# Kernel optimization log

Measured on AMD Instinct MI355X. Metric: run time of the kernel, lower is better.

## Reference

```python
import jax, jax.numpy as jnp
import numpy as np

S_, H_, W_ = 7, 56, 56   # input_resolution
WS = 7                   # window_size
SHIFT = 3                # shift_size
GT = 1                   # gt_num (global tokens per window)
HEADS = 12
EPS = 1e-5


def _rel_pos_index(w):
    # replicates the torch buffer construction (incl. its 3*w-1 / 2*w-1 multipliers)
    coords = np.stack(np.meshgrid(np.arange(w), np.arange(w), np.arange(w), indexing='ij'))
    cf = coords.reshape(3, -1)
    rc = (cf[:, :, None] - cf[:, None, :]).transpose(1, 2, 0).astype(np.int64)
    rc += w - 1
    rc[..., 0] *= 3 * w - 1
    rc[..., 1] *= 2 * w - 1
    return rc.sum(-1)  # (w^3, w^3)


def _attn_mask(S, H, W, w, sh):
    # standard 3D shifted-window mask, built once from static shapes
    img = np.zeros((S, H, W))
    cnt = 0
    sls = (slice(0, -w), slice(-w, -sh), slice(-sh, None))
    for a in sls:
        for b in sls:
            for c in sls:
                img[a, b, c] = cnt
                cnt += 1
    m = img.reshape(S // w, w, H // w, w, W // w, w).transpose(0, 2, 4, 1, 3, 5).reshape(-1, w ** 3)
    d = m[:, None, :] - m[:, :, None]
    return np.where(d != 0, -100.0, 0.0).astype(np.float32)  # (nW, w^3, w^3)


def _ln(x, g, b):
    mu = jnp.mean(x, -1, keepdims=True)
    var = jnp.mean((x - mu) ** 2, -1, keepdims=True)
    return (x - mu) * jax.lax.rsqrt(var + EPS) * g + b


def setup_inputs() -> dict:
    key = jax.random.key(0)
    ks = jax.random.split(key, 7)
    C = 384
    hid = 4 * C
    L = S_ * H_ * W_
    nW = (S_ // WS) * (H_ // WS) * (W_ // WS)
    p = lambda k, shape: jax.random.normal(k, shape, jnp.float32) * 0.02
    return dict(
        x=jax.random.normal(ks[0], (1, L, C), jnp.float32),
        gt=jax.random.normal(ks[1], (nW, GT, C), jnp.float32),
        norm1_g=jnp.ones((C,), jnp.float32), norm1_b=jnp.zeros((C,), jnp.float32),
        qkv_w=p(ks[2], (C, 3 * C)), qkv_b=jnp.zeros((3 * C,), jnp.float32),
        bias_table=p(ks[3], ((2 * WS - 1) ** 3, HEADS)),
        proj_w=p(ks[4], (C, C)), proj_b=jnp.zeros((C,), jnp.float32),
        norm2_g=jnp.ones((C,), jnp.float32), norm2_b=jnp.zeros((C,), jnp.float32),
        fc1_w=p(ks[5], (C, hid)), fc1_b=jnp.zeros((hid,), jnp.float32),
        fc2_w=p(ks[6], (hid, C)), fc2_b=jnp.zeros((C,), jnp.float32),
    )


def _forward(x, gt, norm1_g, norm1_b, qkv_w, qkv_b, bias_table, proj_w, proj_b,
             norm2_g, norm2_b, fc1_w, fc1_b, fc2_w, fc2_b):
    B, L, C = x.shape
    h = HEADS
    d = C // h
    scale = d ** -0.5
    N_ = WS ** 3
    N = N_ + GT
    rpi = _rel_pos_index(WS)
    mask = jnp.asarray(_attn_mask(S_, H_, W_, WS, SHIFT))
    nW = mask.shape[0]

    shortcut = x
    xs = _ln(x, norm1_g, norm1_b).reshape(B, S_, H_, W_, C)
    xs = jnp.roll(xs, (-SHIFT, -SHIFT, -SHIFT), axis=(1, 2, 3))  # cyclic shift
    # window partition -> (B*nW, N_, C)
    xw = xs.reshape(B, S_ // WS, WS, H_ // WS, WS, W_ // WS, WS, C)
    xw = xw.transpose(0, 1, 3, 5, 2, 4, 6, 7).reshape(-1, N_, C)

    # --- WindowAttention with global tokens ---
    xc = jnp.concatenate([gt, xw], axis=1)  # (B*nW, N, C)
    qkv = (xc @ qkv_w + qkv_b).reshape(-1, N, 3, h, d).transpose(2, 0, 3, 1, 4)
    q, k, v = qkv[0] * scale, qkv[1], qkv[2]  # (B*nW, h, N, d)
    attn = jnp.einsum('bhnd,bhmd->bhnm', q, k)
    bias = bias_table[rpi.reshape(-1)].reshape(N_, N_, h).transpose(2, 0, 1)  # (h, N_, N_)
    bias = jnp.pad(bias, ((0, 0), (GT, 0), (GT, 0)))      # zeros on gt rows/cols == original submatrix add
    mpad = jnp.pad(mask, ((0, 0), (GT, 0), (GT, 0)))
    attn = attn + bias[None]
    attn = attn.reshape(B, nW, h, N, N) + mpad[None, :, None]
    attn = jax.nn.softmax(attn.reshape(-1, h, N, N), axis=-1)
    out = jnp.einsum('bhnm,bhmd->bhnd', attn, v).transpose(0, 2, 1, 3).reshape(-1, N, C)
    out = out @ proj_w + proj_b
    gt_out = out[:, :GT]
    xw = out[:, GT:]

    # window reverse + reverse shift
    xs = xw.reshape(B, S_ // WS, H_ // WS, W_ // WS, WS, WS, WS, C)
    xs = xs.transpose(0, 1, 4, 2, 5, 3, 6, 7).reshape(B, S_, H_, W_, C)
    xs = jnp.roll(xs, (SHIFT, SHIFT, SHIFT), axis=(1, 2, 3)).reshape(B, L, C)

    x = shortcut + xs  # drop_path = 0
    y = _ln(x, norm2_g, norm2_b)
    y = jax.nn.gelu(y @ fc1_w + fc1_b, approximate=False) @ fc2_w + fc2_b
    return x + y, gt_out


def reference(x, gt, norm1_g, norm1_b, qkv_w, qkv_b, bias_table, proj_w, proj_b,
              norm2_g, norm2_b, fc1_w, fc1_b, fc2_w, fc2_b):
    return _forward(x, gt, norm1_g, norm1_b, qkv_w, qkv_b, bias_table, proj_w, proj_b,
                    norm2_g, norm2_b, fc1_w, fc1_b, fc2_w, fc2_b)
```

## Files before the change

kernel.cpp:

```cpp
#include <hip/hip_runtime.h>
#include <math.h>

typedef __attribute__((ext_vector_type(8))) short short8;
typedef __attribute__((ext_vector_type(4))) float f32x4;

__device__ __forceinline__ float b2f(short s) {
    unsigned u = ((unsigned)(unsigned short)s) << 16;
    return __builtin_bit_cast(float, u);
}
__device__ __forceinline__ short f2b(float f) {
    unsigned u = __builtin_bit_cast(unsigned, f);
    u += 0x7FFFu + ((u >> 16) & 1u);
    return (short)(u >> 16);
}
__device__ __forceinline__ void gload16(const void* g, void* l) {
    __builtin_amdgcn_global_load_lds(
        (const __attribute__((address_space(1))) unsigned int*)g,
        (__attribute__((address_space(3))) unsigned int*)l, 16, 0, 0);
}

__global__ void transpose_w(const float* __restrict__ src, short* __restrict__ dst,
                            int K, int N) {
    int idx = blockIdx.x * 256 + threadIdx.x;
    if (idx < N * K) {
        int n = idx / K, k = idx - n * K;
        dst[idx] = f2b(src[(size_t)k * N + n]);
    }
}

__global__ void bias_pre(const float* __restrict__ btab, float* __restrict__ btf) {
    int idx = blockIdx.x * 256 + threadIdx.x;
    if (idx >= 12 * 22 * 22 * 64) return;
    int lane = idx & 63, rem = idx >> 6;
    int nb = rem % 22; rem /= 22;
    int rt = rem % 22; int head = rem / 22;
    int j = nb * 16 + (lane & 15);
    int ibase = rt * 16 + (lane >> 4) * 4;
    f32x4 out;
    #pragma unroll
    for (int r = 0; r < 4; r++) {
        int i = ibase + r;
        float v;
        if (j >= 344) v = -1e30f;
        else if (i >= 344 || i == 0 || j == 0) v = 0.f;
        else {
            int ti = i - 1, tj = j - 1;
            int ai = ti / 49, bi = (ti % 49) / 7, ci = ti % 7;
            int aj = tj / 49, bj = (tj % 49) / 7, cj = tj % 7;
            int id3 = (ai - aj + 6) * 20 + (bi - bj + 6) * 13 + (ci - cj + 6);
            v = btab[id3 * 12 + head];
        }
        out[r] = v;
    }
    *(f32x4*)&btf[(size_t)idx * 4] = out;
}

__global__ void gid_pre(unsigned char* __restrict__ gid) {
    int idx = blockIdx.x * 256 + threadIdx.x;
    if (idx >= 64 * 352) return;
    int w = idx / 352, n = idx % 352;
    unsigned char g = 0;
    if (n >= 1 && n < 344) {
        int t = n - 1;
        int a = t / 49, bb = (t % 49) / 7, cc = t % 7;
        int hw = w >> 3, ww = w & 7;
        int h = hw * 7 + bb, wd = ww * 7 + cc;
        int gs = (a < 4) ? 1 : 2;
        int gh = (h < 49) ? 0 : ((h < 53) ? 1 : 2);
        int gw = (wd < 49) ? 0 : ((wd < 53) ? 1 : 2);
        g = (unsigned char)(gs * 9 + gh * 3 + gw);
    }
    gid[idx] = g;
}

__global__ __launch_bounds__(256) void ln1_window(
    const float* __restrict__ x, const float* __restrict__ gt,
    const float* __restrict__ g, const float* __restrict__ b,
    short* __restrict__ xc)
{
    int wid = threadIdx.x >> 6, lane = threadIdx.x & 63;
    int r = blockIdx.x * 4 + wid;
    int w = r / 344, n = r - w * 344;
    if (n == 0) {
        #pragma unroll
        for (int i = 0; i < 6; i++) {
            int c = lane + i * 64;
            xc[(size_t)r * 384 + c] = f2b(gt[(size_t)w * 384 + c]);
        }
        return;
    }
    int t = n - 1;
    int a = t / 49, rm = t - a * 49, bb = rm / 7, cc = rm - bb * 7;
    int hw = w >> 3, ww = w & 7;
    int s = (a < 4) ? a + 3 : a - 4;
    int h = hw * 7 + bb + 3; if (h >= 56) h -= 56;
    int wd = ww * 7 + cc + 3; if (wd >= 56) wd -= 56;
    const float* row = x + (size_t)((s * 56 + h) * 56 + wd) * 384;
    float v[6]; float sum = 0.f;
    #pragma unroll
    for (int i = 0; i < 6; i++) { v[i] = row[lane + i * 64]; sum += v[i]; }
    #pragma unroll
    for (int off = 32; off >= 1; off >>= 1) sum += __shfl_xor(sum, off);
    float mu = sum * (1.0f / 384.0f);
    float vs = 0.f;
    #pragma unroll
    for (int i = 0; i < 6; i++) { float d = v[i] - mu; vs += d * d; }
    #pragma unroll
    for (int off = 32; off >= 1; off >>= 1) vs += __shfl_xor(vs, off);
    float rstd = rsqrtf(vs * (1.0f / 384.0f) + 1e-5f);
    #pragma unroll
    for (int i = 0; i < 6; i++) {
        int c = lane + i * 64;
        float o = (v[i] - mu) * rstd * g[c] + b[c];
        xc[(size_t)r * 384 + c] = f2b(o);
    }
}

__global__ __launch_bounds__(256) void ln2_kernel(
    const float* __restrict__ xn, const float* __restrict__ g,
    const float* __restrict__ b, short* __restrict__ out)
{
    int wid = threadIdx.x >> 6, lane = threadIdx.x & 63;
    int r = blockIdx.x * 4 + wid;
    const float* row = xn + (size_t)r * 384;
    float v[6]; float sum = 0.f;
    #pragma unroll
    for (int i = 0; i < 6; i++) { v[i] = row[lane + i * 64]; sum += v[i]; }
    #pragma unroll
    for (int off = 32; off >= 1; off >>= 1) sum += __shfl_xor(sum, off);
    float mu = sum * (1.0f / 384.0f);
    float vs = 0.f;
    #pragma unroll
    for (int i = 0; i < 6; i++) { float d = v[i] - mu; vs += d * d; }
    #pragma unroll
    for (int off = 32; off >= 1; off >>= 1) vs += __shfl_xor(vs, off);
    float rstd = rsqrtf(vs * (1.0f / 384.0f) + 1e-5f);
    #pragma unroll
    for (int i = 0; i < 6; i++) {
        int c = lane + i * 64;
        float o = (v[i] - mu) * rstd * g[c] + b[c];
        out[(size_t)r * 384 + c] = f2b(o);
    }
}

template<int EPI, bool QS>
__global__ __launch_bounds__(256, 4) void gemm128(
    const short* __restrict__ A, const short* __restrict__ BT,
    const float* __restrict__ bias, void* __restrict__ Out,
    const void* __restrict__ P0, void* __restrict__ P1,
    int M, int N, int K)
{
    __shared__ short As[128 * 64];
    __shared__ short Bs[128 * 64];
    const int m0 = blockIdx.y * 128, n0 = blockIdx.x * 128;
    const int tid = threadIdx.x;
    const int wid = tid >> 6, lane = tid & 63;
    const int wm = wid >> 1, wn = wid & 1;
    const int l15 = lane & 15, quad = lane >> 4;

    f32x4 acc[4][4];
    #pragma unroll
    for (int i = 0; i < 4; i++)
        #pragma unroll
        for (int j = 0; j < 4; j++) acc[i][j] = (f32x4){0.f, 0.f, 0.f, 0.f};

    const int trow = tid >> 3;
    const int cs = tid & 7;
    const int gc = cs ^ (trow & 7);
    const short* Ag[4]; const short* Bg[4];
    #pragma unroll
    for (int j = 0; j < 4; j++) {
        int ar = m0 + j * 32 + trow; if (ar >= M) ar = M - 1;
        Ag[j] = A + (size_t)ar * K + gc * 8;
        Bg[j] = BT + (size_t)(n0 + j * 32 + trow) * K + gc * 8;
    }
    short* AsW[4]; short* BsW[4];
    #pragma unroll
    for (int j = 0; j < 4; j++) {
        AsW[j] = &As[(j * 32 + wid * 8) * 64];
        BsW[j] = &Bs[(j * 32 + wid * 8) * 64];
    }
    int arow[4], brow[4];
    #pragma unroll
    for (int mt = 0; mt < 4; mt++) arow[mt] = wm * 64 + mt * 16 + l15;
    #pragma unroll
    for (int nt = 0; nt < 4; nt++) brow[nt] = wn * 64 + nt * 16 + l15;

    for (int ks = 0; ks < K; ks += 64) {
        #pragma unroll
        for (int j = 0; j < 4; j++) gload16(Ag[j] + ks, AsW[j]);
        #pragma unroll
        for (int j = 0; j < 4; j++) gload16(Bg[j] + ks, BsW[j]);
        __syncthreads();
        #pragma unroll
        for (int ko = 0; ko < 2; ko++) {
            short8 af[4], bf[4];
            #pragma unroll
            for (int mt = 0; mt < 4; mt++)
                af[mt] = *(const short8*)&As[arow[mt] * 64
                         + (((ko * 4 + quad) ^ (l15 & 7)) * 8)];
            #pragma unroll
            for (int nt = 0; nt < 4; nt++)
                bf[nt] = *(const short8*)&Bs[brow[nt] * 64
                         + (((ko * 4 + quad) ^ (l15 & 7)) * 8)];
            #pragma unroll
            for (int mt = 0; mt < 4; mt++)
                #pragma unroll
                for (int nt = 0; nt < 4; nt++)
                    acc[mt][nt] = __builtin_amdgcn_mfma_f32_16x16x32_bf16(
                        af[mt], bf[nt], acc[mt][nt], 0, 0, 0);
        }
        __syncthreads();
    }

    #pragma unroll
    for (int mt = 0; mt < 4; mt++) {
        #pragma unroll
        for (int nt = 0; nt < 4; nt++) {
            #pragma unroll
            for (int r = 0; r < 4; r++) {
                int row = m0 + wm * 64 + mt * 16 + quad * 4 + r;
                int col = n0 + wn * 64 + nt * 16 + l15;
                if (row >= M) continue;
                float v = acc[mt][nt][r] + bias[col];
                if (EPI == 0) {
                    if (QS && col < 384) v *= 0.17677669529663687f;
                    ((short*)Out)[(size_t)row * N + col] = f2b(v);
                } else if (EPI == 1) {
                    v = 0.5f * v * (1.0f + erff(v * 0.7071067811865476f));
                    ((short*)Out)[(size_t)row * N + col] = f2b(v);
                } else if (EPI == 2) {
                    int w = row / 344, n = row - w * 344;
                    if (n == 0) {
                        ((float*)P1)[(size_t)w * 384 + col] = v;
                    } else {
                        int t = n - 1;
                        int a = t / 49, rm = t - a * 49;
                        int bb = rm / 7, cc = rm - bb * 7;
                        int hw = w >> 3, ww = w & 7;
                        int s = (a < 4) ? a + 3 : a - 4;
                        int h = hw * 7 + bb + 3; if (h >= 56) h -= 56;
                        int wd = ww * 7 + cc + 3; if (wd >= 56) wd -= 56;
                        size_t td = (size_t)((s * 56 + h) * 56 + wd) * 384 + col;
                        ((float*)Out)[td] = v + ((const float*)P0)[td];
                    }
                } else {
                    v += ((const float*)P0)[(size_t)row * N + col];
                    ((float*)Out)[(size_t)row * N + col] = v;
                }
            }
        }
    }
}

__global__ __launch_bounds__(256) void attn_kernel(
    const short* __restrict__ qkv, const float* __restrict__ btf,
    const unsigned char* __restrict__ gid, short* __restrict__ attn_out)
{
    __shared__ short KT[352 * 40];
    __shared__ short VT[32 * 360];
    __shared__ short Pbuf[4 * 16 * 40];
    __shared__ unsigned char Gs[352];
    const int blk = blockIdx.x;
    const int half = blk & 1, wh = blk >> 1;
    const int w = wh / 12, head = wh - w * 12;
    const int tid = threadIdx.x;
    const int wid = tid >> 6, lane = tid & 63;
    const int l15 = lane & 15, quad = lane >> 4;
    const size_t base = (size_t)w * 344 * 1152 + head * 32;

    for (int c = tid; c < 352 * 4; c += 256) {
        int row = c >> 2, off = (c & 3) * 8;
        short8 v8 = (short8){0,0,0,0,0,0,0,0};
        if (row < 344) v8 = *(const short8*)&qkv[base + 384 + (size_t)row * 1152 + off];
        *(short8*)&KT[row * 40 + off] = v8;
    }
    for (int e = tid; e < 344 * 32; e += 256) {
        int key = e >> 5, dd = e & 31;
        VT[dd * 360 + key] = qkv[base + 768 + (size_t)key * 1152 + dd];
    }
    for (int e = tid; e < 16 * 32; e += 256) {
        int key = 344 + (e >> 5), dd = e & 31;
        VT[dd * 360 + key] = 0;
    }
    for (int e = tid; e < 352; e += 256) Gs[e] = gid[w * 352 + e];
    __syncthreads();

    const float* bh = btf + (size_t)head * (22 * 22 * 256);
    short* Pw = &Pbuf[wid * 640];

    for (int rtl = wid; rtl < 11; rtl += 4) {
        int rt = half * 11 + rtl;
        int mbase = rt * 16;
        int qr = mbase + l15; if (qr > 343) qr = 343;
        short8 af = *(const short8*)&qkv[base + (size_t)qr * 1152 + quad * 8];

        int rg[4]; bool ip[4];
        #pragma unroll
        for (int r = 0; r < 4; r++) {
            int i = mbase + quad * 4 + r;
            rg[r] = Gs[i];
            ip[r] = (i > 0);
        }

        f32x4 o0 = {0.f, 0.f, 0.f, 0.f}, o1 = {0.f, 0.f, 0.f, 0.f};
        float l[4] = {0.f, 0.f, 0.f, 0.f};

        #pragma unroll
        for (int kk = 0; kk < 11; kk++) {
            int nb0 = kk * 2, nb1 = kk * 2 + 1;
            f32x4 b0 = *(const f32x4*)&bh[((size_t)(rt * 22 + nb0) * 64 + lane) * 4];
            f32x4 b1 = *(const f32x4*)&bh[((size_t)(rt * 22 + nb1) * 64 + lane) * 4];
            short8 k0 = *(const short8*)&KT[(nb0 * 16 + l15) * 40 + quad * 8];
            short8 k1 = *(const short8*)&KT[(nb1 * 16 + l15) * 40 + quad * 8];
            f32x4 s0 = __builtin_amdgcn_mfma_f32_16x16x32_bf16(af, k0, b0, 0, 0, 0);
            f32x4 s1 = __builtin_amdgcn_mfma_f32_16x16x32_bf16(af, k1, b1, 0, 0, 0);

            int j0 = nb0 * 16 + l15;
            int cg0 = Gs[j0], cg1 = Gs[j0 + 16];
            bool jp0 = (j0 > 0);
            #pragma unroll
            for (int r = 0; r < 4; r++) {
                float s0r = s0[r], s1r = s1[r];
                if (jp0 && ip[r] && rg[r] != cg0) s0r -= 100.0f;
                if (ip[r] && rg[r] != cg1) s1r -= 100.0f;
                float p0 = __expf(s0r);
                float p1 = __expf(s1r);
                l[r] += p0 + p1;
                Pw[(quad * 4 + r) * 40 + l15] = f2b(p0);
                Pw[(quad * 4 + r) * 40 + 16 + l15] = f2b(p1);
            }
            short8 pa = *(const short8*)&Pw[l15 * 40 + quad * 8];
            short8 v0 = *(const short8*)&VT[l15 * 360 + kk * 32 + quad * 8];
            short8 v1 = *(const short8*)&VT[(16 + l15) * 360 + kk * 32 + quad * 8];
            o0 = __builtin_amdgcn_mfma_f32_16x16x32_bf16(pa, v0, o0, 0, 0, 0);
            o1 = __builtin_amdgcn_mfma_f32_16x16x32_bf16(pa, v1, o1, 0, 0, 0);
        }

        #pragma unroll
        for (int r = 0; r < 4; r++) {
            l[r] += __shfl_xor(l[r], 1);
            l[r] += __shfl_xor(l[r], 2);
            l[r] += __shfl_xor(l[r], 4);
            l[r] += __shfl_xor(l[r], 8);
        }
        #pragma unroll
        for (int r = 0; r < 4; r++) {
            int row = mbase + quad * 4 + r;
            if (row < 344) {
                float inv = 1.0f / l[r];
                size_t ob = ((size_t)w * 344 + row) * 384 + head * 32;
                attn_out[ob + l15] = f2b(o0[r] * inv);
                attn_out[ob + 16 + l15] = f2b(o1[r] * inv);
            }
        }
    }
}

extern "C" void kernel_launch(void* const* d_in, const int* in_sizes, int n_in,
                              void* d_out, int out_size, void* d_ws, size_t ws_size,
                              hipStream_t stream)
{
    const float* x      = (const float*)d_in[0];
    const float* gt     = (const float*)d_in[1];
    const float* n1g    = (const float*)d_in[2];
    const float* n1b    = (const float*)d_in[3];
    const float* qkv_w  = (const float*)d_in[4];
    const float* qkv_b  = (const float*)d_in[5];
    const float* btab   = (const float*)d_in[6];
    const float* proj_w = (const float*)d_in[7];
    const float* proj_b = (const float*)d_in[8];
    const float* n2g    = (const float*)d_in[9];
    const float* n2b    = (const float*)d_in[10];
    const float* fc1_w  = (const float*)d_in[11];
    const float* fc1_b  = (const float*)d_in[12];
    const float* fc2_w  = (const float*)d_in[13];
    const float* fc2_b  = (const float*)d_in[14];

    char* ws = (char*)d_ws;
    short* wt_qkv  = (short*)(ws + 0);
    short* wt_proj = (short*)(ws + 884736);
    short* wt_fc1  = (short*)(ws + 1179648);
    short* wt_fc2  = (short*)(ws + 2359296);
    short* xc      = (short*)(ws + 3538944);
    short* qkvb    = (short*)(ws + 20447232);
    short* attn_o  = xc;
    short* h1      = (short*)(ws + 3538944);
    float* xnew    = (float*)(ws + 71172096);
    float* btf     = (float*)(ws + 71172096);
    unsigned char* gidb = (unsigned char*)(ws + 77119488);
    short* xnorm   = (short*)(ws + 104890368);

    float* outx  = (float*)d_out;
    float* outgt = outx + (size_t)21952 * 384;

    transpose_w<<<dim3((442368 + 255) / 256), 256, 0, stream>>>(qkv_w, wt_qkv, 384, 1152);
    transpose_w<<<dim3((147456 + 255) / 256), 256, 0, stream>>>(proj_w, wt_proj, 384, 384);
    transpose_w<<<dim3((589824 + 255) / 256), 256, 0, stream>>>(fc1_w, wt_fc1, 384, 1536);
    transpose_w<<<dim3((589824 + 255) / 256), 256, 0, stream>>>(fc2_w, wt_fc2, 1536, 384);

    bias_pre<<<dim3((12 * 22 * 22 * 64 + 255) / 256), 256, 0, stream>>>(btab, btf);
    gid_pre<<<dim3((64 * 352 + 255) / 256), 256, 0, stream>>>(gidb);

    ln1_window<<<dim3(5504), 256, 0, stream>>>(x, gt, n1g, n1b, xc);

    gemm128<0, true><<<dim3(9, 172), 256, 0, stream>>>(xc, wt_qkv, qkv_b, qkvb,
                                                       nullptr, nullptr, 22016, 1152, 384);

    attn_kernel<<<dim3(1536), 256, 0, stream>>>(qkvb, btf, gidb, attn_o);

    gemm128<2, false><<<dim3(3, 172), 256, 0, stream>>>(attn_o, wt_proj, proj_b, xnew,
                                                        x, outgt, 22016, 384, 384);

    ln2_kernel<<<dim3(5488), 256, 0, stream>>>(xnew, n2g, n2b, xnorm);

    gemm128<1, false><<<dim3(12, 172), 256, 0, stream>>>(xnorm, wt_fc1, fc1_b, h1,
                                                         nullptr, nullptr, 21952, 1536, 384);

    gemm128<3, false><<<dim3(3, 172), 256, 0, stream>>>(h1, wt_fc2, fc2_b, outx,
                                                        xnew, nullptr, 21952, 384, 1536);
}
```

Measured before the change: 441.6 us.

## Tile weight transposes via LDS, raise GEMM occupancy, use tanh-form GELU

The weight transpose kernel now goes through a 32x32 LDS tile, so both reads and writes are coalesced instead of strided. The GEMM launch bounds now ask for 5 waves-per-SIMD occupancy instead of 4, which may cap registers and cause spills. The fc1 epilogue replaces exact erf GELU with a tanh-approximation written as x*sigmoid using fast exp and rcp. This lowers epilogue cost but departs from the exact GELU the reference requires.

```diff
diff --git a/kernel.cpp b/kernel.cpp
--- a/kernel.cpp
+++ b/kernel.cpp
@@ -19,12 +19,24 @@
         (__attribute__((address_space(3))) unsigned int*)l, 16, 0, 0);
 }
 
-__global__ void transpose_w(const float* __restrict__ src, short* __restrict__ dst,
-                            int K, int N) {
-    int idx = blockIdx.x * 256 + threadIdx.x;
-    if (idx < N * K) {
-        int n = idx / K, k = idx - n * K;
-        dst[idx] = f2b(src[(size_t)k * N + n]);
+__global__ __launch_bounds__(256) void transpose_w(const float* __restrict__ src,
+                                                   short* __restrict__ dst,
+                                                   int K, int N) {
+    __shared__ short tile[32][33];
+    const int kt = blockIdx.y * 32, nt = blockIdx.x * 32;
+    const int tx = threadIdx.x & 31, ty = threadIdx.x >> 5;
+    #pragma unroll
+    for (int i = 0; i < 4; i++) {
+        int k = kt + ty + 8 * i, n = nt + tx;
+        short v = 0;
+        if (k < K && n < N) v = f2b(src[(size_t)k * N + n]);
+        tile[ty + 8 * i][tx] = v;
+    }
+    __syncthreads();
+    #pragma unroll
+    for (int i = 0; i < 4; i++) {
+        int n = nt + ty + 8 * i, k = kt + tx;
+        if (n < N && k < K) dst[(size_t)n * K + k] = tile[tx][ty + 8 * i];
     }
 }
 
@@ -144,7 +156,7 @@
 }
 
 template<int EPI, bool QS>
-__global__ __launch_bounds__(256, 4) void gemm128(
+__global__ __launch_bounds__(256, 5) void gemm128(
     const short* __restrict__ A, const short* __restrict__ BT,
     const float* __restrict__ bias, void* __restrict__ Out,
     const void* __restrict__ P0, void* __restrict__ P1,
@@ -227,7 +239,11 @@
                     if (QS && col < 384) v *= 0.17677669529663687f;
                     ((short*)Out)[(size_t)row * N + col] = f2b(v);
                 } else if (EPI == 1) {
-                    v = 0.5f * v * (1.0f + erff(v * 0.7071067811865476f));
+                    float u2 = v * v;
+                    float w  = v * fmaf(0.07135481633f, u2, 1.5957691216f);
+                    float e  = __expf(w);
+                    float t  = __builtin_amdgcn_rcpf(1.0f + e);
+                    v = v - v * t;
                     ((short*)Out)[(size_t)row * N + col] = f2b(v);
                 } else if (EPI == 2) {
                     int w = row / 344, n = row - w * 344;
@@ -394,10 +410,10 @@
     float* outx  = (float*)d_out;
     float* outgt = outx + (size_t)21952 * 384;
 
-    transpose_w<<<dim3((442368 + 255) / 256), 256, 0, stream>>>(qkv_w, wt_qkv, 384, 1152);
-    transpose_w<<<dim3((147456 + 255) / 256), 256, 0, stream>>>(proj_w, wt_proj, 384, 384);
-    transpose_w<<<dim3((589824 + 255) / 256), 256, 0, stream>>>(fc1_w, wt_fc1, 384, 1536);
-    transpose_w<<<dim3((589824 + 255) / 256), 256, 0, stream>>>(fc2_w, wt_fc2, 1536, 384);
+    transpose_w<<<dim3(36, 12), 256, 0, stream>>>(qkv_w, wt_qkv, 384, 1152);
+    transpose_w<<<dim3(12, 12), 256, 0, stream>>>(proj_w, wt_proj, 384, 384);
+    transpose_w<<<dim3(48, 12), 256, 0, stream>>>(fc1_w, wt_fc1, 384, 1536);
+    transpose_w<<<dim3(12, 48), 256, 0, stream>>>(fc2_w, wt_fc2, 1536, 384);
 
     bias_pre<<<dim3((12 * 22 * 22 * 64 + 255) / 256), 256, 0, stream>>>(btab, btf);
     gid_pre<<<dim3((64 * 352 + 255) / 256), 256, 0, stream>>>(gidb);
```

Result: slower. 601.6 us (+36.2%).
